# Performance work log

Measured on AMD Instinct MI355X. Metric: run time of the kernel, lower is better.

The kernel has to match this reference:

```python
import jax, jax.numpy as jnp
import numpy as np
from jax import lax

# Solver hyper-params for the smoothed robust-OT LP (fixed-iteration, jit-safe)
N_STEPS = 60
TAU = 0.05    # softmax temperature smoothing max over classes
RHO = 10.0    # quadratic penalty weight on the Wasserstein-cost constraint
LR = 0.5


def setup_inputs() -> dict:
    key = jax.random.key(0)
    ks = jax.random.split(key, 6)
    X = jax.random.normal(ks[0], (16, 96, 3, 64, 64), jnp.float32)
    Qr = jax.random.uniform(ks[1], (16, 10, 96), jnp.float32) + 0.1
    Q = Qr / Qr.sum(-1, keepdims=True)  # each (b,k) row is a distribution over samples
    conv_w = jax.random.normal(ks[2], (32, 3, 3, 3), jnp.float32) * 0.05
    conv_b = jnp.zeros((32,), jnp.float32)
    fc_w = jax.random.normal(ks[3], (256, 30752), jnp.float32) * 0.01
    fc_b = jnp.zeros((256,), jnp.float32)
    theta = jnp.ones((10,), jnp.float32) * 0.1
    return {"X": X, "Q": Q, "conv_w": conv_w, "conv_b": conv_b,
            "fc_w": fc_w, "fc_b": fc_b, "theta": theta}


def _features(X, conv_w, conv_b, fc_w, fc_b):
    B, S = X.shape[:2]
    x = X.reshape(B * S, *X.shape[2:])  # [B*S, C, H, W]
    x = lax.conv_general_dilated(x, conv_w, window_strides=(1, 1), padding='VALID',
                                 dimension_numbers=('NCHW', 'OIHW', 'NCHW'))
    x = jax.nn.relu(x + conv_b[None, :, None, None])
    x = lax.reduce_window(x, -jnp.inf, lax.max, (1, 1, 2, 2), (1, 1, 2, 2), 'VALID')
    # dropout is identity in eval mode
    x = x.reshape(B * S, -1)
    x = jax.nn.relu(x @ fc_w.T + fc_b)
    return x.reshape(B, S, -1)  # [B, S, F]


def _pairwise_sqdist(feats):
    n2 = (feats ** 2).sum(-1)  # [B, S]
    D = n2[:, :, None] + n2[:, None, :] - 2.0 * jnp.einsum('bif,bjf->bij', feats, feats)
    diag = jnp.diagonal(D, axis1=1, axis2=2)  # [B, S]
    return jnp.clip(D - diag[:, None, :], 0.0)


def _robust_ot_solve(D, Q, theta):
    # Approximate the CvxpyLayer LP:
    #   min_gamma sum_l max_k p_k[l]  s.t. gamma_k rows sum to Q_k, <gamma_k, C> <= theta_k
    # via mirror-descent on a row-stochastic parameterization (rows of gamma_k are
    # Q_k[i]-scaled softmaxes), with a smoothed max (logsumexp) and quadratic penalty.
    B, K, S = Q.shape

    def obj(A):
        gamma = Q[..., None] * jax.nn.softmax(A, axis=-1)      # [B,K,S,S]
        p = gamma.sum(axis=2)                                   # column sums [B,K,S]
        smooth_max = TAU * jax.nn.logsumexp(p / TAU, axis=1)    # [B,S]
        cost = jnp.einsum('bkij,bij->bk', gamma, D)             # [B,K]
        pen = jnp.sum(jax.nn.relu(cost - theta[None, :]) ** 2)
        return smooth_max.sum() + RHO * pen

    grad_obj = jax.grad(obj)

    @jax.checkpoint
    def step(A, _):
        return A - LR * grad_obj(A), None

    A0 = jnp.zeros((B, K, S, S), D.dtype)
    A, _ = lax.scan(step, A0, None, length=N_STEPS)
    gamma = Q[..., None] * jax.nn.softmax(A, axis=-1)
    return gamma.sum(axis=2)  # p_hat [B,K,S]


def reference(X, Q, conv_w, conv_b, fc_w, fc_b, theta):
    feats = _features(X, conv_w, conv_b, fc_w, fc_b)   # [B,S,F]
    D = _pairwise_sqdist(feats)                        # [B,S,S]
    p_hat = _robust_ot_solve(D, Q, theta)              # [B,K,S]
    return p_hat
```

## Files before the change

### kernel.cpp

```cpp
#include <hip/hip_runtime.h>

#define BB 16
#define SS 96
#define KK 10
#define FF 256
#define IH 64
#define IW 64
#define OCH 32
#define PH 31
#define PW 31
#define NPOS 961
#define FDIM 30752
#define NIMG 1536

#define TAUI 20.0f
#define RHOC 10.0f
#define LRC  0.5f
#define NSTEPS 60

#define KSPLIT 31
#define KCHE 992

#define WCBLK ((FF * FDIM) / 1024)

typedef _Float16 v8hf __attribute__((ext_vector_type(8)));
typedef _Float16 v4hf __attribute__((ext_vector_type(4)));
typedef __fp16 h2 __attribute__((ext_vector_type(2)));
typedef float v4f __attribute__((ext_vector_type(4)));

__global__ __launch_bounds__(256)
void prep(const float* __restrict__ X, const float* __restrict__ convw,
          const float* __restrict__ bias, _Float16* __restrict__ pooled,
          const float* __restrict__ fcw, _Float16* __restrict__ wh) {
    const int tid = threadIdx.x;
    if (blockIdx.x >= NIMG) {
        const size_t i = ((size_t)(blockIdx.x - NIMG) * 256 + tid) * 4;
        float4 v = *(const float4*)(fcw + i);
        v4hf o = {(_Float16)v.x, (_Float16)v.y, (_Float16)v.z, (_Float16)v.w};
        *(v4hf*)(wh + i) = o;
        return;
    }
    __shared__ _Float16 Xl[3 * 64 * 64 + 256];
    __shared__ _Float16 Wl[32 * 32];
    const int img = blockIdx.x;
    const float* xb = X + (size_t)img * (3 * IH * IW);
#pragma unroll
    for (int i = 0; i < 12; i++) {
        const int e = tid + i * 256;
        float4 v = *(const float4*)(xb + (size_t)e * 4);
        h2 p0 = __builtin_amdgcn_cvt_pkrtz(v.x, v.y);
        h2 p1 = __builtin_amdgcn_cvt_pkrtz(v.z, v.w);
        *(h2*)&Xl[e * 4] = p0;
        *(h2*)&Xl[e * 4 + 2] = p1;
    }
    for (int t = tid; t < 1024; t += 256) {
        const int oc = t >> 5, k = t & 31;
        Wl[t] = (k < 27) ? (_Float16)convw[oc * 27 + k] : (_Float16)0.f;
    }
    __syncthreads();

    const int lane = tid & 63;
    const int l16 = lane & 15, q = lane >> 4;
    const int wv = tid >> 6;
    v8hf a0 = *(const v8hf*)&Wl[l16 * 32 + q * 8];
    v8hf a1 = *(const v8hf*)&Wl[(16 + l16) * 32 + q * 8];
    int off[8];
#pragma unroll
    for (int j = 0; j < 8; j++) {
        const int k = q * 8 + j;
        const int c = k / 9, rem = k - c * 9;
        const int ky = rem / 3, kx = rem - ky * 3;
        off[j] = c * 4096 + ky * 64 + kx;
    }
    const bool hi_ok = (q < 3);
    float b0r[4], b1r[4];
#pragma unroll
    for (int i = 0; i < 4; i++) {
        b0r[i] = bias[q * 4 + i];
        b1r[i] = bias[16 + q * 4 + i];
    }
    _Float16* outp = pooled + (size_t)img * FDIM;

    for (int oy = wv; oy < PH; oy += 4) {
        const int y0 = oy * 2;
#pragma unroll
        for (int xt = 0; xt < 4; xt++) {
            const int x = xt * 16 + l16;
            const int base0 = y0 * 64 + x;
            v8hf bf0, bf1;
#pragma unroll
            for (int j = 0; j < 8; j++) {
                _Float16 h0 = Xl[base0 + off[j]];
                _Float16 h1 = Xl[base0 + 64 + off[j]];
                if (j >= 3 && !hi_ok) { h0 = (_Float16)0.f; h1 = (_Float16)0.f; }
                bf0[j] = h0; bf1[j] = h1;
            }
            v4f c00 = (v4f)(0.f), c10 = (v4f)(0.f), c01 = (v4f)(0.f), c11 = (v4f)(0.f);
            c00 = __builtin_amdgcn_mfma_f32_16x16x32_f16(a0, bf0, c00, 0, 0, 0);
            c10 = __builtin_amdgcn_mfma_f32_16x16x32_f16(a1, bf0, c10, 0, 0, 0);
            c01 = __builtin_amdgcn_mfma_f32_16x16x32_f16(a0, bf1, c01, 0, 0, 0);
            c11 = __builtin_amdgcn_mfma_f32_16x16x32_f16(a1, bf1, c11, 0, 0, 0);
            const int ox = xt * 8 + (l16 >> 1);
            const bool act = ((l16 & 1) == 0) && (ox < PW);
#pragma unroll
            for (int i = 0; i < 4; i++) {
                float m0 = fmaxf(c00[i], c01[i]);
                float m1 = fmaxf(c10[i], c11[i]);
                m0 = fmaxf(m0, __shfl_xor(m0, 1));
                m1 = fmaxf(m1, __shfl_xor(m1, 1));
                if (act) {
                    const int oc0 = q * 4 + i;
                    const float r0 = fmaxf(m0 + b0r[i], 0.f);
                    const float r1 = fmaxf(m1 + b1r[i], 0.f);
                    outp[(size_t)oc0 * NPOS + oy * PW + ox] = (_Float16)r0;
                    outp[(size_t)(16 + oc0) * NPOS + oy * PW + ox] = (_Float16)r1;
                }
            }
        }
    }
}

__global__ __launch_bounds__(256)
void fc_gemm(const _Float16* __restrict__ Ah, const _Float16* __restrict__ Wh,
             float* __restrict__ fpart) {
    __shared__ _Float16 Asl[128 * 56];
    __shared__ _Float16 Bsl[128 * 56];
    const int m0 = blockIdx.x * 128, n0 = blockIdx.y * 128;
    const int k0 = blockIdx.z * KCHE;
    const int tid = threadIdx.x;
    const int wave = tid >> 6, lane = tid & 63;
    const int quad = lane >> 4, l16 = lane & 15;
    const int wm = (wave & 1) * 64, wn = (wave >> 1) * 64;
    const int ar = tid >> 1, ac = (tid & 1) * 16;
    const _Float16* Ag = Ah + (size_t)(m0 + ar) * FDIM + ac;
    const _Float16* Bg = Wh + (size_t)(n0 + ar) * FDIM + ac;

    v4f acc[4][4];
#pragma unroll
    for (int i = 0; i < 4; i++)
#pragma unroll
        for (int j = 0; j < 4; j++) acc[i][j] = (v4f)(0.f);

    for (int s = 0; s < KCHE / 32; s++) {
        const int gk = k0 + (s << 5);
        uint4 a0 = *(const uint4*)(Ag + gk);
        uint4 a1 = *(const uint4*)(Ag + gk + 8);
        uint4 b0 = *(const uint4*)(Bg + gk);
        uint4 b1 = *(const uint4*)(Bg + gk + 8);
        __syncthreads();
        *(uint4*)&Asl[ar * 56 + ac] = a0;
        *(uint4*)&Asl[ar * 56 + ac + 8] = a1;
        *(uint4*)&Bsl[ar * 56 + ac] = b0;
        *(uint4*)&Bsl[ar * 56 + ac + 8] = b1;
        __syncthreads();
        v8hf af[4], bf[4];
#pragma unroll
        for (int mt = 0; mt < 4; mt++)
            af[mt] = *(const v8hf*)&Asl[(wm + mt * 16 + l16) * 56 + quad * 8];
#pragma unroll
        for (int nt = 0; nt < 4; nt++)
            bf[nt] = *(const v8hf*)&Bsl[(wn + nt * 16 + l16) * 56 + quad * 8];
#pragma unroll
        for (int mt = 0; mt < 4; mt++)
#pragma unroll
            for (int nt = 0; nt < 4; nt++)
                acc[mt][nt] = __builtin_amdgcn_mfma_f32_16x16x32_f16(
                    af[mt], bf[nt], acc[mt][nt], 0, 0, 0);
    }
    float* outz = fpart + (size_t)blockIdx.z * NIMG * FF;
#pragma unroll
    for (int mt = 0; mt < 4; mt++)
#pragma unroll
        for (int nt = 0; nt < 4; nt++)
#pragma unroll
            for (int i = 0; i < 4; i++) {
                const int gm = m0 + wm + mt * 16 + quad * 4 + i;
                const int gn = n0 + wn + nt * 16 + l16;
                outz[(size_t)gm * FF + gn] = acc[mt][nt][i];
            }
}

__global__ __launch_bounds__(256)
void bias_sum_relu(const float* __restrict__ fpart, const float* __restrict__ bias,
                   float* __restrict__ f, float* __restrict__ n2) {
    const int tid = threadIdx.x;
    const size_t idx = ((size_t)blockIdx.x * 256 + tid) * 4;
    float4 s = make_float4(0.f, 0.f, 0.f, 0.f);
#pragma unroll
    for (int z = 0; z < KSPLIT; z++) {
        float4 v = *(const float4*)(fpart + (size_t)z * NIMG * FF + idx);
        s.x += v.x; s.y += v.y; s.z += v.z; s.w += v.w;
    }
    const int col = (int)(idx & (FF - 1));
    float4 bv = *(const float4*)(bias + col);
    float4 o;
    o.x = fmaxf(s.x + bv.x, 0.f);
    o.y = fmaxf(s.y + bv.y, 0.f);
    o.z = fmaxf(s.z + bv.z, 0.f);
    o.w = fmaxf(s.w + bv.w, 0.f);
    *(float4*)(f + idx) = o;
    float sq = o.x * o.x + o.y * o.y + o.z * o.z + o.w * o.w;
#pragma unroll
    for (int mm = 32; mm >= 1; mm >>= 1) sq += __shfl_xor(sq, mm);
    if ((tid & 63) == 0) n2[blockIdx.x * 4 + (tid >> 6)] = sq;
}

__global__ __launch_bounds__(256)
void dmat(const float* __restrict__ feats, const float* __restrict__ n2,
          float* __restrict__ Dm) {
    const int i0 = blockIdx.x * 16, j0 = blockIdx.y * 16, b = blockIdx.z;
    __shared__ float fi[16][260], fj[16][260];
    const int tid = threadIdx.x;
    const int r = tid >> 4, c0 = (tid & 15) * 16;
    const float* fbase = feats + (size_t)b * SS * FF;
#pragma unroll
    for (int v = 0; v < 16; v += 4) {
        float4 a = *(const float4*)(fbase + (size_t)(i0 + r) * FF + c0 + v);
        float4 w = *(const float4*)(fbase + (size_t)(j0 + r) * FF + c0 + v);
        *(float4*)&fi[r][c0 + v] = a;
        *(float4*)&fj[r][c0 + v] = w;
    }
    __syncthreads();
    const int ti = tid >> 4, tj = tid & 15;
    float dot = 0.f;
#pragma unroll 4
    for (int f = 0; f < FF; f += 4) {
        float4 a = *(const float4*)&fi[ti][f];
        float4 w = *(const float4*)&fj[tj][f];
        dot += a.x * w.x + a.y * w.y + a.z * w.z + a.w * w.w;
    }
    const int i = i0 + ti, j = j0 + tj;
    const float d = n2[b * SS + i] + n2[b * SS + j] - 2.f * dot;
    Dm[((size_t)b * SS + i) * SS + j] = fmaxf(d, 0.f);
}

__global__ __launch_bounds__(512)
void ot_kernel(const float* __restrict__ Dg, const float* __restrict__ Qg,
               const float* __restrict__ thetag, float* __restrict__ ppub,
               unsigned* __restrict__ bar, float* __restrict__ out) {
    const int bk = blockIdx.x;
    const int b = bk % BB, k = bk / BB;
    const int tid = threadIdx.x;
    const int hw = tid >> 5, l = tid & 31;

    __shared__ float ppart[16][SS];
    __shared__ float cpart[16];
    __shared__ float Msh[SS];
    __shared__ float pown[SS];
    __shared__ float costsh, lamsh;

    float a[6][3], e[6][3], dre[6][3], rz[6], qi[6];

    const float* Db = Dg + (size_t)b * SS * SS;
    const float* Qb = Qg + ((size_t)b * KK + k) * SS;
#pragma unroll
    for (int r = 0; r < 6; r++) {
        const int i = hw * 6 + r;
#pragma unroll
        for (int u = 0; u < 3; u++) dre[r][u] = Db[i * SS + l + 32 * u];
        qi[r] = Qb[i];
    }
    const float th = thetag[k];
    unsigned* ctr = bar + b * 64;
    unsigned target = 0;

    auto publish_and_wait = [&](int buf) {
        if (tid < SS)
            __hip_atomic_store(&ppub[(((size_t)buf * BB + b) * KK + k) * SS + tid],
                               pown[tid], __ATOMIC_RELAXED, __HIP_MEMORY_SCOPE_AGENT);
        asm volatile("s_waitcnt vmcnt(0)" ::: "memory");
        __syncthreads();
        target += KK;
        if (tid == 0) {
            __hip_atomic_fetch_add(ctr, 1u, __ATOMIC_RELAXED, __HIP_MEMORY_SCOPE_AGENT);
            while (__hip_atomic_load(ctr, __ATOMIC_RELAXED, __HIP_MEMORY_SCOPE_AGENT) < target)
                __builtin_amdgcn_s_sleep(2);
        }
        __syncthreads();
    };

    auto collect = [&]() {
        __syncthreads();
        if (tid < SS) {
            float s = 0.f;
#pragma unroll
            for (int h = 0; h < 16; h++) s += ppart[h][tid];
            pown[tid] = s;
        }
        if (tid == 0) {
            float c = 0.f;
#pragma unroll
            for (int h = 0; h < 16; h++) c += cpart[h];
            costsh = c;
            lamsh = 2.f * RHOC * fmaxf(c - th, 0.f);
        }
        __syncthreads();
    };

    {
        float cd[6];
#pragma unroll
        for (int r = 0; r < 6; r++) {
#pragma unroll
            for (int u = 0; u < 3; u++) { a[r][u] = 0.f; e[r][u] = 1.f; }
            rz[r] = 1.f / 96.f;
            cd[r] = dre[r][0] + dre[r][1] + dre[r][2];
        }
#pragma unroll
        for (int mm = 16; mm >= 1; mm >>= 1)
#pragma unroll
            for (int r = 0; r < 6; r++) cd[r] += __shfl_xor(cd[r], mm);
        float pp0 = 0.f, cc = 0.f;
#pragma unroll
        for (int r = 0; r < 6; r++) {
            const float scale = qi[r] * rz[r];
            pp0 += scale;
            cc += scale * cd[r];
        }
        ppart[hw][l] = pp0; ppart[hw][l + 32] = pp0; ppart[hw][l + 64] = pp0;
        if (l == 0) cpart[hw] = cc;
        collect();
    }
    publish_and_wait(0);

    for (int t = 0; t < NSTEPS; t++) {
        const int rbuf = t & 1;
        if (tid < SS) {
            const float* ps = ppub + (((size_t)rbuf * BB + b) * KK) * SS + tid;
            float v[KK];
            float mx = -1e30f;
#pragma unroll
            for (int kk2 = 0; kk2 < KK; kk2++) {
                v[kk2] = __hip_atomic_load(&ps[kk2 * SS], __ATOMIC_RELAXED,
                                           __HIP_MEMORY_SCOPE_AGENT) * TAUI;
                mx = fmaxf(mx, v[kk2]);
            }
            float sum = 0.f;
#pragma unroll
            for (int kk2 = 0; kk2 < KK; kk2++) sum += __expf(v[kk2] - mx);
            Msh[tid] = __expf(v[k] - mx) * __builtin_amdgcn_rcpf(sum);
        }
        __syncthreads();
        const float lam = lamsh;
        const float M0 = Msh[l], M1 = Msh[l + 32], M2 = Msh[l + 64];

        float g[6][3], dt[6];
#pragma unroll
        for (int r = 0; r < 6; r++) {
            g[r][0] = fmaf(lam, dre[r][0], M0);
            g[r][1] = fmaf(lam, dre[r][1], M1);
            g[r][2] = fmaf(lam, dre[r][2], M2);
            dt[r] = (e[r][0] * g[r][0] + e[r][1] * g[r][1] + e[r][2] * g[r][2]) * rz[r];
        }
#pragma unroll
        for (int mm = 16; mm >= 1; mm >>= 1)
#pragma unroll
            for (int r = 0; r < 6; r++) dt[r] += __shfl_xor(dt[r], mm);

        float mrow[6];
#pragma unroll
        for (int r = 0; r < 6; r++) {
            const float cq = LRC * qi[r] * rz[r];
            a[r][0] -= cq * e[r][0] * (g[r][0] - dt[r]);
            a[r][1] -= cq * e[r][1] * (g[r][1] - dt[r]);
            a[r][2] -= cq * e[r][2] * (g[r][2] - dt[r]);
            mrow[r] = fmaxf(a[r][0], fmaxf(a[r][1], a[r][2]));
        }
#pragma unroll
        for (int mm = 16; mm >= 1; mm >>= 1)
#pragma unroll
            for (int r = 0; r < 6; r++) mrow[r] = fmaxf(mrow[r], __shfl_xor(mrow[r], mm));

        float zz[6], cd[6];
#pragma unroll
        for (int r = 0; r < 6; r++) {
            e[r][0] = __expf(a[r][0] - mrow[r]);
            e[r][1] = __expf(a[r][1] - mrow[r]);
            e[r][2] = __expf(a[r][2] - mrow[r]);
            zz[r] = e[r][0] + e[r][1] + e[r][2];
            cd[r] = e[r][0] * dre[r][0] + e[r][1] * dre[r][1] + e[r][2] * dre[r][2];
        }
#pragma unroll
        for (int mm = 16; mm >= 1; mm >>= 1)
#pragma unroll
            for (int r = 0; r < 6; r++) {
                zz[r] += __shfl_xor(zz[r], mm);
                cd[r] += __shfl_xor(cd[r], mm);
            }

        float pp0 = 0.f, pp1 = 0.f, pp2 = 0.f, cc = 0.f;
#pragma unroll
        for (int r = 0; r < 6; r++) {
            const float rzz = __builtin_amdgcn_rcpf(zz[r]);
            rz[r] = rzz;
            const float scale = qi[r] * rzz;
            pp0 += scale * e[r][0];
            pp1 += scale * e[r][1];
            pp2 += scale * e[r][2];
            cc += scale * cd[r];
        }
        ppart[hw][l] = pp0; ppart[hw][l + 32] = pp1; ppart[hw][l + 64] = pp2;
        if (l == 0) cpart[hw] = cc;
        collect();
        if (t < NSTEPS - 1) publish_and_wait((t + 1) & 1);
    }
    if (tid < SS) out[((size_t)b * KK + k) * SS + tid] = pown[tid];
}

extern "C" void kernel_launch(void* const* d_in, const int* in_sizes, int n_in,
                              void* d_out, int out_size, void* d_ws, size_t ws_size,
                              hipStream_t stream) {
    const float* X     = (const float*)d_in[0];
    const float* Q     = (const float*)d_in[1];
    const float* convw = (const float*)d_in[2];
    const float* convb = (const float*)d_in[3];
    const float* fcw   = (const float*)d_in[4];
    const float* fcb   = (const float*)d_in[5];
    const float* theta = (const float*)d_in[6];
    float* out = (float*)d_out;

    char* ws = (char*)d_ws;
    size_t off = 0;
    auto take = [&](size_t nbytes) {
        char* p = ws + off;
        off += (nbytes + 255) & ~(size_t)255;
        return (void*)p;
    };
    _Float16* pooled = (_Float16*)take((size_t)NIMG * FDIM * 2);
    _Float16* Wh     = (_Float16*)take((size_t)FF * FDIM * 2);
    float*    fpart  = (float*)take((size_t)KSPLIT * NIMG * FF * 4);
    float*    feats  = (float*)take((size_t)NIMG * FF * 4);
    float*    n2     = (float*)take((size_t)NIMG * 4);
    float*    Dm     = (float*)take((size_t)BB * SS * SS * 4);
    float*    ppub   = (float*)take((size_t)2 * BB * KK * SS * 4);
    unsigned* bar    = (unsigned*)take((size_t)BB * 64 * 4);

    (void)hipMemsetAsync(bar, 0, (size_t)BB * 64 * 4, stream);

    hipLaunchKernelGGL(prep, dim3(NIMG + WCBLK), dim3(256), 0, stream,
                       X, convw, convb, pooled, fcw, Wh);
    hipLaunchKernelGGL(fc_gemm, dim3(12, 2, KSPLIT), dim3(256), 0, stream, pooled, Wh, fpart);
    hipLaunchKernelGGL(bias_sum_relu, dim3(NIMG * FF / 1024), dim3(256), 0, stream,
                       fpart, fcb, feats, n2);
    hipLaunchKernelGGL(dmat, dim3(6, 6, BB), dim3(256), 0, stream, feats, n2, Dm);
    hipLaunchKernelGGL(ot_kernel, dim3(BB * KK), dim3(512), 0, stream, Dm, Q, theta, ppub, bar, out);
}
```

Baseline: 525.7 us.

## Pack two OT classes per block to halve grid-barrier participants

The OT solver now runs two k-classes per 1024-thread block (80 blocks instead of 160). Each block's two halves share the per-step reductions through shared memory, and the partner's column sums are read locally instead of from global memory. The global per-batch barrier counter now waits for 5 arrivals instead of 10. This cuts barrier traffic and global atomic loads per step, but it doubles block size, which raises register pressure and reduces how many blocks can be resident at once.

```diff
diff --git a/kernel.cpp b/kernel.cpp
--- a/kernel.cpp
+++ b/kernel.cpp
@@ -234,20 +234,25 @@
     Dm[((size_t)b * SS + i) * SS + j] = fmaxf(d, 0.f);
 }
 
-__global__ __launch_bounds__(512)
+__global__ __launch_bounds__(1024)
 void ot_kernel(const float* __restrict__ Dg, const float* __restrict__ Qg,
                const float* __restrict__ thetag, float* __restrict__ ppub,
                unsigned* __restrict__ bar, float* __restrict__ out) {
     const int bk = blockIdx.x;
-    const int b = bk % BB, k = bk / BB;
+    const int b = bk % BB;
+    const int kp = bk / BB;
     const int tid = threadIdx.x;
-    const int hw = tid >> 5, l = tid & 31;
-
-    __shared__ float ppart[16][SS];
-    __shared__ float cpart[16];
-    __shared__ float Msh[SS];
-    __shared__ float pown[SS];
-    __shared__ float costsh, lamsh;
+    const int sub = tid >> 9;
+    const int t5 = tid & 511;
+    const int k = kp + sub * 5;
+    const int kpart = kp + (1 - sub) * 5;
+    const int hw = t5 >> 5, l = t5 & 31;
+
+    __shared__ float ppart[2][16][SS];
+    __shared__ float cpart[2][16];
+    __shared__ float Msh[2][SS];
+    __shared__ float pown[2][SS];
+    __shared__ float lamsh[2];
 
     float a[6][3], e[6][3], dre[6][3], rz[6], qi[6];
 
@@ -265,12 +270,12 @@
     unsigned target = 0;
 
     auto publish_and_wait = [&](int buf) {
-        if (tid < SS)
-            __hip_atomic_store(&ppub[(((size_t)buf * BB + b) * KK + k) * SS + tid],
-                               pown[tid], __ATOMIC_RELAXED, __HIP_MEMORY_SCOPE_AGENT);
+        if (t5 < SS)
+            __hip_atomic_store(&ppub[(((size_t)buf * BB + b) * KK + k) * SS + t5],
+                               pown[sub][t5], __ATOMIC_RELAXED, __HIP_MEMORY_SCOPE_AGENT);
         asm volatile("s_waitcnt vmcnt(0)" ::: "memory");
         __syncthreads();
-        target += KK;
+        target += 5;
         if (tid == 0) {
             __hip_atomic_fetch_add(ctr, 1u, __ATOMIC_RELAXED, __HIP_MEMORY_SCOPE_AGENT);
             while (__hip_atomic_load(ctr, __ATOMIC_RELAXED, __HIP_MEMORY_SCOPE_AGENT) < target)
@@ -281,18 +286,17 @@
 
     auto collect = [&]() {
         __syncthreads();
-        if (tid < SS) {
+        if (t5 < SS) {
             float s = 0.f;
 #pragma unroll
-            for (int h = 0; h < 16; h++) s += ppart[h][tid];
-            pown[tid] = s;
-        }
-        if (tid == 0) {
+            for (int h = 0; h < 16; h++) s += ppart[sub][h][t5];
+            pown[sub][t5] = s;
+        }
+        if (t5 == 0) {
             float c = 0.f;
 #pragma unroll
-            for (int h = 0; h < 16; h++) c += cpart[h];
-            costsh = c;
-            lamsh = 2.f * RHOC * fmaxf(c - th, 0.f);
+            for (int h = 0; h < 16; h++) c += cpart[sub][h];
+            lamsh[sub] = 2.f * RHOC * fmaxf(c - th, 0.f);
         }
         __syncthreads();
     };
@@ -317,32 +321,40 @@
             pp0 += scale;
             cc += scale * cd[r];
         }
-        ppart[hw][l] = pp0; ppart[hw][l + 32] = pp0; ppart[hw][l + 64] = pp0;
-        if (l == 0) cpart[hw] = cc;
+        ppart[sub][hw][l] = pp0; ppart[sub][hw][l + 32] = pp0; ppart[sub][hw][l + 64] = pp0;
+        if (l == 0) cpart[sub][hw] = cc;
         collect();
     }
     publish_and_wait(0);
 
     for (int t = 0; t < NSTEPS; t++) {
         const int rbuf = t & 1;
-        if (tid < SS) {
-            const float* ps = ppub + (((size_t)rbuf * BB + b) * KK) * SS + tid;
+        if (t5 < SS) {
+            const float* ps = ppub + (((size_t)rbuf * BB + b) * KK) * SS + t5;
+            const float vown = pown[sub][t5] * TAUI;
             float v[KK];
+#pragma unroll
+            for (int kk2 = 0; kk2 < KK; kk2++) {
+                if (kk2 == k) {
+                    v[kk2] = vown;
+                } else if (kk2 == kpart) {
+                    v[kk2] = pown[1 - sub][t5] * TAUI;
+                } else {
+                    v[kk2] = __hip_atomic_load(&ps[(size_t)kk2 * SS], __ATOMIC_RELAXED,
+                                               __HIP_MEMORY_SCOPE_AGENT) * TAUI;
+                }
+            }
             float mx = -1e30f;
 #pragma unroll
-            for (int kk2 = 0; kk2 < KK; kk2++) {
-                v[kk2] = __hip_atomic_load(&ps[kk2 * SS], __ATOMIC_RELAXED,
-                                           __HIP_MEMORY_SCOPE_AGENT) * TAUI;
-                mx = fmaxf(mx, v[kk2]);
-            }
+            for (int kk2 = 0; kk2 < KK; kk2++) mx = fmaxf(mx, v[kk2]);
             float sum = 0.f;
 #pragma unroll
             for (int kk2 = 0; kk2 < KK; kk2++) sum += __expf(v[kk2] - mx);
-            Msh[tid] = __expf(v[k] - mx) * __builtin_amdgcn_rcpf(sum);
-        }
-        __syncthreads();
-        const float lam = lamsh;
-        const float M0 = Msh[l], M1 = Msh[l + 32], M2 = Msh[l + 64];
+            Msh[sub][t5] = __expf(vown - mx) * __builtin_amdgcn_rcpf(sum);
+        }
+        __syncthreads();
+        const float lam = lamsh[sub];
+        const float M0 = Msh[sub][l], M1 = Msh[sub][l + 32], M2 = Msh[sub][l + 64];
 
         float g[6][3], dt[6];
 #pragma unroll
@@ -399,12 +411,12 @@
             pp2 += scale * e[r][2];
             cc += scale * cd[r];
         }
-        ppart[hw][l] = pp0; ppart[hw][l + 32] = pp1; ppart[hw][l + 64] = pp2;
-        if (l == 0) cpart[hw] = cc;
+        ppart[sub][hw][l] = pp0; ppart[sub][hw][l + 32] = pp1; ppart[sub][hw][l + 64] = pp2;
+        if (l == 0) cpart[sub][hw] = cc;
         collect();
         if (t < NSTEPS - 1) publish_and_wait((t + 1) & 1);
     }
-    if (tid < SS) out[((size_t)b * KK + k) * SS + tid] = pown[tid];
+    if (t5 < SS) out[((size_t)b * KK + k) * SS + t5] = pown[sub][t5];
 }
 
 extern "C" void kernel_launch(void* const* d_in, const int* in_sizes, int n_in,
@@ -443,5 +455,6 @@
     hipLaunchKernelGGL(bias_sum_relu, dim3(NIMG * FF / 1024), dim3(256), 0, stream,
                        fpart, fcb, feats, n2);
     hipLaunchKernelGGL(dmat, dim3(6, 6, BB), dim3(256), 0, stream, feats, n2, Dm);
-    hipLaunchKernelGGL(ot_kernel, dim3(BB * KK), dim3(512), 0, stream, Dm, Q, theta, ppub, bar, out);
-}
+    hipLaunchKernelGGL(ot_kernel, dim3(BB * KK / 2), dim3(1024), 0, stream,
+                       Dm, Q, theta, ppub, bar, out);
+}
```

Result: slower. 784.6 us (+49.3%).
